# Optimization experiments

Measured on AMD Instinct MI355X. Metric: run time of the kernel, lower is better.

Reference implementation:

```python
import jax, jax.numpy as jnp
import numpy as np

IOU_HI = 0.5
IOU_LO = 0.0
ROI_BS = 256
POS_RATIO = 0.25
BG = 20  # background class id; valid classes 0..BG-1
NUM_POS = int(ROI_BS * POS_RATIO)
DELTAS_SCALING = np.array([10.0, 10.0, 5.0, 5.0], dtype=np.float32)  # (x, y, w, h)


def _make_boxes(key, shape):
    ka, kb = jax.random.split(key)
    c = jax.random.uniform(ka, shape + (2,), minval=0.05, maxval=0.95)
    s = jax.random.uniform(kb, shape + (2,), minval=0.02, maxval=0.4)
    lo = jnp.clip(c - s / 2, 0.0, 1.0)
    hi = jnp.clip(c + s / 2, 0.0, 1.0)
    return jnp.concatenate([lo, hi], -1)  # (y1, x1, y2, x2), normalized


def setup_inputs() -> dict:
    key = jax.random.key(0)
    k1, k2, k3 = jax.random.split(key, 3)
    B, N, G = 32, 12000, 200
    rois = _make_boxes(k1, (B, N))
    gt_boxes = _make_boxes(k2, (B, G))
    # class == BG marks a padded / invalid GT box
    gt_class_ids = jax.random.randint(k3, (B, G), 0, BG + 1).astype(jnp.int32)
    return {"rois": rois, "gt_class_ids": gt_class_ids, "gt_boxes": gt_boxes}


def _iou(rois, gts):
    # rois [N,4], gts [G,4] in (y1,x1,y2,x2) -> [N,G]
    y1 = jnp.maximum(rois[:, None, 0], gts[None, :, 0])
    x1 = jnp.maximum(rois[:, None, 1], gts[None, :, 1])
    y2 = jnp.minimum(rois[:, None, 2], gts[None, :, 2])
    x2 = jnp.minimum(rois[:, None, 3], gts[None, :, 3])
    inter = jnp.clip(y2 - y1, 0.0) * jnp.clip(x2 - x1, 0.0)
    ar = (rois[:, 2] - rois[:, 0]) * (rois[:, 3] - rois[:, 1])
    ag = (gts[:, 2] - gts[:, 0]) * (gts[:, 3] - gts[:, 1])
    return inter / (ar[:, None] + ag[None, :] - inter + 1e-8)


def _encode(r, g):
    # (tx, ty, tw, th) * scaling, r/g: [K,4] in (y1,x1,y2,x2)
    eps = 1e-6
    rh = r[:, 2] - r[:, 0]; rw = r[:, 3] - r[:, 1]
    rcy = r[:, 0] + rh / 2; rcx = r[:, 1] + rw / 2
    gh = g[:, 2] - g[:, 0]; gw = g[:, 3] - g[:, 1]
    gcy = g[:, 0] + gh / 2; gcx = g[:, 1] + gw / 2
    tx = (gcx - rcx) / (rw + eps)
    ty = (gcy - rcy) / (rh + eps)
    tw = jnp.log(jnp.maximum(gw, eps) / (rw + eps))
    th = jnp.log(jnp.maximum(gh, eps) / (rh + eps))
    return jnp.stack([tx, ty, tw, th], -1) * jnp.asarray(DELTAS_SCALING)


def _per_image(rois, gt_cls, gt_boxes):
    iou = _iou(rois, gt_boxes)                       # [N,G]
    valid_gt = gt_cls < BG
    iou = jnp.where(valid_gt[None, :], iou, -1.0)
    max_iou = iou.max(1)                             # [N]
    best_gt = iou.argmax(1)                          # [N]
    pos = max_iou >= IOU_HI
    neg = (max_iou < IOU_HI) & (max_iou >= IOU_LO)

    # deterministic sampling: highest-IoU positives / negatives first
    pos_val, pos_idx = jax.lax.top_k(jnp.where(pos, max_iou, -1.0), NUM_POS)
    pos_ok = pos_val > 0.0
    neg_val, neg_idx = jax.lax.top_k(jnp.where(neg, max_iou + 2.0, -1.0), ROI_BS)
    neg_ok = neg_val > 0.0

    rP = jnp.arange(NUM_POS, dtype=jnp.float32)
    rN = jnp.arange(ROI_BS, dtype=jnp.float32)
    prio = jnp.concatenate([jnp.where(pos_ok, 1e9 - rP, -1e9 - rP),
                            jnp.where(neg_ok, 1e6 - rN, -1e6 - rN)])
    cand_idx = jnp.concatenate([pos_idx, neg_idx])
    cand_pos = jnp.concatenate([pos_ok, jnp.zeros(ROI_BS, bool)])
    _, sel = jax.lax.top_k(prio, ROI_BS)
    sel_roi = cand_idx[sel]                          # [ROI_BS]
    sel_is_pos = cand_pos[sel]                       # [ROI_BS]

    labels = jnp.where(sel_is_pos, gt_cls[best_gt[sel_roi]], BG)
    rois_sel = rois[sel_roi]                         # [ROI_BS,4]
    gts_sel = gt_boxes[best_gt[sel_roi]]             # [ROI_BS,4]
    t = _encode(rois_sel, gts_sel) * sel_is_pos[:, None].astype(rois.dtype)

    cls_onehot = jax.nn.one_hot(labels, BG + 1, dtype=rois.dtype)   # [ROI_BS,BG+1]
    onehot_fg = jax.nn.one_hot(labels, BG, dtype=rois.dtype)        # zero row for bg
    mask4 = jnp.repeat(onehot_fg, 4, axis=1)                        # [ROI_BS,4*BG]
    deltas_full = (onehot_fg[:, :, None] * t[:, None, :]).reshape(ROI_BS, 4 * BG)
    reg = jnp.concatenate([mask4, deltas_full], -1)                 # [ROI_BS,8*BG]
    return rois_sel, cls_onehot, reg


def reference(rois, gt_class_ids, gt_boxes):
    return jax.vmap(_per_image)(rois, gt_class_ids, gt_boxes)
```

## Files before the change

### kernel.cpp

```cpp
#include <hip/hip_runtime.h>
#include <stdint.h>

#pragma clang fp contract(off)

#define BATCH 32
#define NROI  12000
#define NGT   200
#define BGCLS 20
#define ROIBS 256
#define NPOS  64
#define NBIN  1024
#define CAP   1024
#define TSEL  1024
#define HSH   16
#define HST   (NBIN + 2)

__device__ __forceinline__ void roi_maxiou_all(const float4* cbox, const float* carea,
                                               int nv, float ry1, float rx1,
                                               float ry2, float rx2,
                                               float& best, int& bj) {
#pragma clang fp contract(off)
  float ar = (ry2 - ry1) * (rx2 - rx1);
  best = -1.0f; bj = 0;
  for (int j = 0; j < nv; ++j) {
    float4 q = cbox[j];
    float yy1 = fmaxf(ry1, q.x);
    float xx1 = fmaxf(rx1, q.y);
    float yy2 = fminf(ry2, q.z);
    float xx2 = fminf(rx2, q.w);
    float inter = fmaxf(yy2 - yy1, 0.0f) * fmaxf(xx2 - xx1, 0.0f);
    float den = ((ar + carea[j]) - inter) + 1e-8f;
    float iou = inter / den;
    if (iou > best) { best = iou; bj = j; }
  }
}

__global__ __launch_bounds__(256) void k_ioumax(const float* __restrict__ rois,
                                                const int* __restrict__ gtc,
                                                const float* __restrict__ gtb,
                                                float* __restrict__ max_iou,
                                                int* __restrict__ best_j) {
#pragma clang fp contract(off)
  __shared__ float4 cbox[NGT];
  __shared__ float carea[NGT];
  __shared__ int snv, wtmp[4];
  const int b = blockIdx.y;
  const int tid = threadIdx.x;

  {
    bool valid = false; float4 p = make_float4(0.f, 0.f, 0.f, 0.f);
    if (tid < NGT) {
      p = *(const float4*)(gtb + ((size_t)b * NGT + tid) * 4);
      valid = gtc[(size_t)b * NGT + tid] < BGCLS;
    }
    unsigned long long m = __ballot(valid);
    int w = tid >> 6;
    if ((tid & 63) == 0) wtmp[w] = __popcll(m);
    __syncthreads();
    if (tid == 0) snv = wtmp[0] + wtmp[1] + wtmp[2] + wtmp[3];
    if (valid) {
      int off = 0;
      for (int i = 0; i < w; ++i) off += wtmp[i];
      int pos = off + __popcll(m & ((1ull << (tid & 63)) - 1ull));
      cbox[pos] = p;
      carea[pos] = (p.z - p.x) * (p.w - p.y);
    }
    __syncthreads();
  }
  const int nv = snv;

  int n = blockIdx.x * 256 + tid;
  if (n >= NROI) return;
  const float4 r = *(const float4*)(rois + ((size_t)b * NROI + n) * 4);
  const float ar = (r.z - r.x) * (r.w - r.y);

  float best; int bj;
  if (nv == 0) {
    best = -1.0f; bj = 0;
  } else {
    float v1 = -1.0f, v2 = -2.0f; int j1 = 0;
#pragma unroll 2
    for (int j = 0; j < nv; ++j) {
      float4 q = cbox[j];
      float ag = carea[j];
      float yy1 = fmaxf(r.x, q.x);
      float xx1 = fmaxf(r.y, q.y);
      float yy2 = fminf(r.z, q.z);
      float xx2 = fminf(r.w, q.w);
      float inter = fmaxf(yy2 - yy1, 0.0f) * fmaxf(xx2 - xx1, 0.0f);
      float den = ((ar + ag) - inter) + 1e-8f;
      float a = inter * __builtin_amdgcn_rcpf(den);
      bool gt = a > v1;
      v2 = gt ? v1 : fmaxf(v2, a);
      j1 = gt ? j : j1;
      v1 = gt ? a : v1;
    }
    if (v2 >= v1 * 0.999995f) {
      roi_maxiou_all(cbox, carea, nv, r.x, r.y, r.z, r.w, best, bj);
    } else {
      float4 q = cbox[j1];
      float yy1 = fmaxf(r.x, q.x);
      float xx1 = fmaxf(r.y, q.y);
      float yy2 = fminf(r.z, q.z);
      float xx2 = fminf(r.w, q.w);
      float inter = fmaxf(yy2 - yy1, 0.0f) * fmaxf(xx2 - xx1, 0.0f);
      float den = ((ar + carea[j1]) - inter) + 1e-8f;
      best = inter / den;
      bj = j1;
    }
  }
  max_iou[(size_t)b * NROI + n] = best;
  best_j[(size_t)b * NROI + n] = bj;
}

template <bool USE_WS>
__global__ __launch_bounds__(TSEL) void k_sel(const float* __restrict__ rois,
                                              const int* __restrict__ gtc,
                                              const float* __restrict__ gtb,
                                              const float* __restrict__ max_iou,
                                              const int* __restrict__ best_j,
                                              float* __restrict__ out) {
#pragma clang fp contract(off)
  __shared__ float4 cbox[NGT];
  __shared__ float carea[NGT];
  __shared__ int ccls[NGT];
  __shared__ int snv, wtmp[16];
  __shared__ int wtot[16], wnext[16];
  __shared__ float val[NROI];
  __shared__ unsigned long long list[CAP];
  __shared__ int hs[HSH][HST];
  __shared__ int ss[NBIN];
  __shared__ int sel_r[ROIBS];
  __shared__ int scnt, sT;
  const int b = blockIdx.x;
  const int tid = threadIdx.x;

  {
    bool valid = false; float4 p = make_float4(0.f, 0.f, 0.f, 0.f); int cls = BGCLS;
    if (tid < NGT) {
      p = *(const float4*)(gtb + ((size_t)b * NGT + tid) * 4);
      cls = gtc[(size_t)b * NGT + tid];
      valid = (cls < BGCLS);
    }
    unsigned long long m = __ballot(valid);
    int w = tid >> 6;
    if ((tid & 63) == 0) wtmp[w] = __popcll(m);
    if (tid < ROIBS) sel_r[tid] = 0;
    __syncthreads();
    if (tid == 0) { int s = 0; for (int i = 0; i < 16; ++i) s += wtmp[i]; snv = s; }
    if (valid) {
      int off = 0;
      for (int i = 0; i < w; ++i) off += wtmp[i];
      int pos = off + __popcll(m & ((1ull << (tid & 63)) - 1ull));
      cbox[pos] = p;
      carea[pos] = (p.z - p.x) * (p.w - p.y);
      ccls[pos] = cls;
    }
    __syncthreads();
  }
  const int nv = snv;

  if constexpr (USE_WS) {
    for (int n = tid; n < NROI; n += TSEL) val[n] = max_iou[(size_t)b * NROI + n];
  } else {
    for (int n = tid; n < NROI; n += TSEL) {
      const float4 r = *(const float4*)(rois + ((size_t)b * NROI + n) * 4);
      float best; int bj;
      roi_maxiou_all(cbox, carea, nv, r.x, r.y, r.z, r.w, best, bj);
      val[n] = best;
    }
  }
  __syncthreads();

  auto phase = [&](bool isPos, int need, unsigned base, int shift,
                   float lo, float hi, int slotBase) -> int {
    for (int i = tid; i < HSH * HST; i += TSEL) ((int*)hs)[i] = 0;
    if (tid == 0) { scnt = 0; sT = 0; }
    __syncthreads();
    const int sh = tid & (HSH - 1);
    for (int n = tid; n < NROI; n += TSEL) {
      float v = val[n];
      if (v >= lo && v < hi) {
        float kv = isPos ? v : (v + 2.0f);
        int bin = min((int)((__float_as_uint(kv) - base) >> shift), NBIN - 1);
        atomicAdd(&hs[sh][bin], 1);
      }
    }
    __syncthreads();
    int cnt_bin = 0;
#pragma unroll
    for (int i = 0; i < HSH; ++i) cnt_bin += hs[i][tid];
    const int lane = tid & 63, w = tid >> 6;
    int sfx = cnt_bin;
#pragma unroll
    for (int off = 1; off < 64; off <<= 1) {
      int t = __shfl_down(sfx, off, 64);
      sfx += (lane + off < 64) ? t : 0;
    }
    if (lane == 0) wtot[w] = sfx;
    __syncthreads();
    if (tid < 16) {
      int s = 0;
      for (int i = tid + 1; i < 16; ++i) s += wtot[i];
      wnext[tid] = s;
    }
    __syncthreads();
    const int suffix = sfx + wnext[w];
    ss[tid] = suffix;
    __syncthreads();
    {
      int nxt = (tid + 1 < NBIN) ? ss[tid + 1] : 0;
      if (suffix >= need && nxt < need) sT = tid;
    }
    __syncthreads();
    const int T = sT;
    for (int n = tid; n < NROI; n += TSEL) {
      float v = val[n];
      if (v >= lo && v < hi) {
        unsigned kh = __float_as_uint(isPos ? v : (v + 2.0f));
        int bin = min((int)((kh - base) >> shift), NBIN - 1);
        if (bin >= T) {
          int idx = atomicAdd(&scnt, 1);
          if (idx < CAP)
            list[idx] = ((unsigned long long)kh << 32) | (unsigned)(0x7fffffff - n);
        }
      }
    }
    __syncthreads();
    const int cnt = min(scnt, CAP);
    const int limit = min(cnt, need);
    if (tid < cnt) {
      unsigned long long ki = list[tid];
      int rank = 0;
      for (int j = 0; j < cnt; ++j) rank += (list[j] > ki);
      if (rank < limit)
        sel_r[slotBase + rank] = 0x7fffffff - (int)(ki & 0xffffffffu);
    }
    __syncthreads();
    return limit;
  };

  const int P = phase(true, NPOS, 0x3F000000u, 13, 0.5f, 3.0f, 0);
  phase(false, ROIBS - P, 0x40000000u, 11, 0.0f, 0.5f, P);

  {
    const int slot = tid >> 2, q = tid & 3;
    const int r = sel_r[slot];
    const int isp = (slot < P) ? 1 : 0;
    const float4 rv = *(const float4*)(rois + ((size_t)b * NROI + r) * 4);
    float ry1 = rv.x, rx1 = rv.y, ry2 = rv.z, rx2 = rv.w;
    int bj;
    if constexpr (USE_WS) {
      bj = best_j[(size_t)b * NROI + r];
    } else {
      float bb;
      roi_maxiou_all(cbox, carea, nv, ry1, rx1, ry2, rx2, bb, bj);
    }
    int label = isp ? ccls[bj] : BGCLS;

    float* out1 = out;
    float* out2 = out + (size_t)BATCH * ROIBS * 4;
    float* out3 = out + (size_t)BATCH * ROIBS * 25;
    size_t row = (size_t)b * ROIBS + slot;

    if (q == 0) {
      *(float4*)(out1 + row * 4) = rv;
      float* o2 = out2 + row * 21;
      for (int c = 0; c <= BGCLS; ++c) o2[c] = (c == label) ? 1.0f : 0.0f;
    }

    float t0 = 0.f, t1 = 0.f, t2 = 0.f, t3 = 0.f;
    if (isp) {
      const float eps = 1e-6f;
      float4 g = cbox[bj];
      float gy1 = g.x, gx1 = g.y, gy2 = g.z, gx2 = g.w;
      float rh = ry2 - ry1, rw = rx2 - rx1;
      float rcy = ry1 + rh * 0.5f, rcx = rx1 + rw * 0.5f;
      float gh = gy2 - gy1, gw = gx2 - gx1;
      float gcy = gy1 + gh * 0.5f, gcx = gx1 + gw * 0.5f;
      t0 = ((gcx - rcx) / (rw + eps)) * 10.0f;
      t1 = ((gcy - rcy) / (rh + eps)) * 10.0f;
      t2 = logf(fmaxf(gw, eps) / (rw + eps)) * 5.0f;
      t3 = logf(fmaxf(gh, eps) / (rh + eps)) * 5.0f;
    }
    int m0 = label * 4;
    float* o3 = out3 + row * 160;
    for (int c = q * 10; c < q * 10 + 10; ++c) {
      float4 wv = make_float4(0.f, 0.f, 0.f, 0.f);
      if (isp) {
        float* wp = &wv.x;
#pragma unroll
        for (int jj = 0; jj < 4; ++jj) {
          int e = c * 4 + jj;
          float x = 0.f;
          if (e >= m0 && e < m0 + 4) x = 1.0f;
          int d = e - 80 - m0;
          if (d == 0) x = t0; else if (d == 1) x = t1;
          else if (d == 2) x = t2; else if (d == 3) x = t3;
          wp[jj] = x;
        }
      }
      *(float4*)(o3 + c * 4) = wv;
    }
  }
}

extern "C" void kernel_launch(void* const* d_in, const int* in_sizes, int n_in,
                              void* d_out, int out_size, void* d_ws, size_t ws_size,
                              hipStream_t stream) {
  const float* rois = (const float*)d_in[0];
  const int*   gtc  = (const int*)d_in[1];
  const float* gtb  = (const float*)d_in[2];
  float*       out  = (float*)d_out;

  size_t need = (size_t)BATCH * NROI * 8;
  if (d_ws && ws_size >= need) {
    float* mi = (float*)d_ws;
    int*   bj = (int*)d_ws + (size_t)BATCH * NROI;
    k_ioumax<<<dim3((NROI + 255) / 256, BATCH), 256, 0, stream>>>(rois, gtc, gtb, mi, bj);
    k_sel<true><<<BATCH, TSEL, 0, stream>>>(rois, gtc, gtb, mi, bj, out);
  } else {
    k_sel<false><<<BATCH, TSEL, 0, stream>>>(rois, gtc, gtb, nullptr, nullptr, out);
  }
}
```

Baseline: 86.33 us.

## Process two ROIs per thread in IoU kernel, keep IoU values in registers

Result: slower. 89.53 us (+3.7%).

```diff
diff --git a/kernel.cpp b/kernel.cpp
--- a/kernel.cpp
+++ b/kernel.cpp
@@ -12,8 +12,11 @@
 #define NBIN  1024
 #define CAP   1024
 #define TSEL  1024
+#define VPT2  12
 #define HSH   16
 #define HST   (NBIN + 2)
+#define RPT   2
+#define IOBLK (256 * RPT)
 
 __device__ __forceinline__ void roi_maxiou_all(const float4* cbox, const float* carea,
                                                int nv, float ry1, float rx1,
@@ -35,11 +38,11 @@
   }
 }
 
-__global__ __launch_bounds__(256) void k_ioumax(const float* __restrict__ rois,
-                                                const int* __restrict__ gtc,
-                                                const float* __restrict__ gtb,
-                                                float* __restrict__ max_iou,
-                                                int* __restrict__ best_j) {
+__global__ __launch_bounds__(256, 4) void k_ioumax(const float* __restrict__ rois,
+                                                   const int* __restrict__ gtc,
+                                                   const float* __restrict__ gtb,
+                                                   float* __restrict__ max_iou,
+                                                   int* __restrict__ best_j) {
 #pragma clang fp contract(off)
   __shared__ float4 cbox[NGT];
   __shared__ float carea[NGT];
@@ -68,49 +71,59 @@
     __syncthreads();
   }
   const int nv = snv;
-
-  int n = blockIdx.x * 256 + tid;
-  if (n >= NROI) return;
-  const float4 r = *(const float4*)(rois + ((size_t)b * NROI + n) * 4);
-  const float ar = (r.z - r.x) * (r.w - r.y);
-
-  float best; int bj;
-  if (nv == 0) {
-    best = -1.0f; bj = 0;
-  } else {
-    float v1 = -1.0f, v2 = -2.0f; int j1 = 0;
+  const int n0 = blockIdx.x * IOBLK + tid;
+
+  float4 rb[RPT]; float ar[RPT]; float v1[RPT], v2[RPT]; int j1[RPT];
+#pragma unroll
+  for (int k = 0; k < RPT; ++k) {
+    int n = n0 + (k << 8);
+    rb[k] = (n < NROI) ? *(const float4*)(rois + ((size_t)b * NROI + n) * 4)
+                       : make_float4(2.f, 2.f, 2.f, 2.f);
+    ar[k] = (rb[k].z - rb[k].x) * (rb[k].w - rb[k].y);
+    v1[k] = -1.0f; v2[k] = -2.0f; j1[k] = 0;
+  }
 #pragma unroll 2
-    for (int j = 0; j < nv; ++j) {
-      float4 q = cbox[j];
-      float ag = carea[j];
-      float yy1 = fmaxf(r.x, q.x);
-      float xx1 = fmaxf(r.y, q.y);
-      float yy2 = fminf(r.z, q.z);
-      float xx2 = fminf(r.w, q.w);
+  for (int j = 0; j < nv; ++j) {
+    float4 q = cbox[j];
+    float ag = carea[j];
+#pragma unroll
+    for (int k = 0; k < RPT; ++k) {
+      float yy1 = fmaxf(rb[k].x, q.x);
+      float xx1 = fmaxf(rb[k].y, q.y);
+      float yy2 = fminf(rb[k].z, q.z);
+      float xx2 = fminf(rb[k].w, q.w);
       float inter = fmaxf(yy2 - yy1, 0.0f) * fmaxf(xx2 - xx1, 0.0f);
-      float den = ((ar + ag) - inter) + 1e-8f;
+      float den = ((ar[k] + ag) - inter) + 1e-8f;
       float a = inter * __builtin_amdgcn_rcpf(den);
-      bool gt = a > v1;
-      v2 = gt ? v1 : fmaxf(v2, a);
-      j1 = gt ? j : j1;
-      v1 = gt ? a : v1;
-    }
-    if (v2 >= v1 * 0.999995f) {
-      roi_maxiou_all(cbox, carea, nv, r.x, r.y, r.z, r.w, best, bj);
+      bool gt = a > v1[k];
+      v2[k] = gt ? v1[k] : fmaxf(v2[k], a);
+      j1[k] = gt ? j : j1[k];
+      v1[k] = gt ? a : v1[k];
+    }
+  }
+#pragma unroll
+  for (int k = 0; k < RPT; ++k) {
+    int n = n0 + (k << 8);
+    if (n >= NROI) continue;
+    float best; int bj;
+    if (nv == 0) {
+      best = -1.0f; bj = 0;
+    } else if (v2[k] >= v1[k] * 0.999995f) {
+      roi_maxiou_all(cbox, carea, nv, rb[k].x, rb[k].y, rb[k].z, rb[k].w, best, bj);
     } else {
-      float4 q = cbox[j1];
-      float yy1 = fmaxf(r.x, q.x);
-      float xx1 = fmaxf(r.y, q.y);
-      float yy2 = fminf(r.z, q.z);
-      float xx2 = fminf(r.w, q.w);
+      float4 q = cbox[j1[k]];
+      float yy1 = fmaxf(rb[k].x, q.x);
+      float xx1 = fmaxf(rb[k].y, q.y);
+      float yy2 = fminf(rb[k].z, q.z);
+      float xx2 = fminf(rb[k].w, q.w);
       float inter = fmaxf(yy2 - yy1, 0.0f) * fmaxf(xx2 - xx1, 0.0f);
-      float den = ((ar + carea[j1]) - inter) + 1e-8f;
+      float den = ((ar[k] + carea[j1[k]]) - inter) + 1e-8f;
       best = inter / den;
-      bj = j1;
-    }
-  }
-  max_iou[(size_t)b * NROI + n] = best;
-  best_j[(size_t)b * NROI + n] = bj;
+      bj = j1[k];
+    }
+    max_iou[(size_t)b * NROI + n] = best;
+    best_j[(size_t)b * NROI + n] = bj;
+  }
 }
 
 template <bool USE_WS>
@@ -126,7 +139,6 @@
   __shared__ int ccls[NGT];
   __shared__ int snv, wtmp[16];
   __shared__ int wtot[16], wnext[16];
-  __shared__ float val[NROI];
   __shared__ unsigned long long list[CAP];
   __shared__ int hs[HSH][HST];
   __shared__ int ss[NBIN];
@@ -134,6 +146,7 @@
   __shared__ int scnt, sT;
   const int b = blockIdx.x;
   const int tid = threadIdx.x;
+  const int lane = tid & 63;
 
   {
     bool valid = false; float4 p = make_float4(0.f, 0.f, 0.f, 0.f); int cls = BGCLS;
@@ -160,17 +173,21 @@
   }
   const int nv = snv;
 
-  if constexpr (USE_WS) {
-    for (int n = tid; n < NROI; n += TSEL) val[n] = max_iou[(size_t)b * NROI + n];
-  } else {
-    for (int n = tid; n < NROI; n += TSEL) {
-      const float4 r = *(const float4*)(rois + ((size_t)b * NROI + n) * 4);
-      float best; int bj;
-      roi_maxiou_all(cbox, carea, nv, r.x, r.y, r.z, r.w, best, bj);
-      val[n] = best;
-    }
-  }
-  __syncthreads();
+  float v[VPT2];
+#pragma unroll
+  for (int i = 0; i < VPT2; ++i) {
+    int n = tid + (i << 10);
+    if constexpr (USE_WS) {
+      v[i] = (n < NROI) ? max_iou[(size_t)b * NROI + n] : -3.0f;
+    } else {
+      if (n < NROI) {
+        const float4 r = *(const float4*)(rois + ((size_t)b * NROI + n) * 4);
+        float best; int bj;
+        roi_maxiou_all(cbox, carea, nv, r.x, r.y, r.z, r.w, best, bj);
+        v[i] = best;
+      } else v[i] = -3.0f;
+    }
+  }
 
   auto phase = [&](bool isPos, int need, unsigned base, int shift,
                    float lo, float hi, int slotBase) -> int {
@@ -178,10 +195,11 @@
     if (tid == 0) { scnt = 0; sT = 0; }
     __syncthreads();
     const int sh = tid & (HSH - 1);
-    for (int n = tid; n < NROI; n += TSEL) {
-      float v = val[n];
-      if (v >= lo && v < hi) {
-        float kv = isPos ? v : (v + 2.0f);
+#pragma unroll
+    for (int i = 0; i < VPT2; ++i) {
+      float x = v[i];
+      if (x >= lo && x < hi) {
+        float kv = isPos ? x : (x + 2.0f);
         int bin = min((int)((__float_as_uint(kv) - base) >> shift), NBIN - 1);
         atomicAdd(&hs[sh][bin], 1);
       }
@@ -190,7 +208,7 @@
     int cnt_bin = 0;
 #pragma unroll
     for (int i = 0; i < HSH; ++i) cnt_bin += hs[i][tid];
-    const int lane = tid & 63, w = tid >> 6;
+    const int w = tid >> 6;
     int sfx = cnt_bin;
 #pragma unroll
     for (int off = 1; off < 64; off <<= 1) {
@@ -214,16 +232,26 @@
     }
     __syncthreads();
     const int T = sT;
-    for (int n = tid; n < NROI; n += TSEL) {
-      float v = val[n];
-      if (v >= lo && v < hi) {
-        unsigned kh = __float_as_uint(isPos ? v : (v + 2.0f));
+#pragma unroll
+    for (int i = 0; i < VPT2; ++i) {
+      int n = tid + (i << 10);
+      float x = v[i];
+      bool pred = (x >= lo && x < hi);
+      unsigned kh = 0; 
+      if (pred) {
+        kh = __float_as_uint(isPos ? x : (x + 2.0f));
         int bin = min((int)((kh - base) >> shift), NBIN - 1);
-        if (bin >= T) {
-          int idx = atomicAdd(&scnt, 1);
-          if (idx < CAP)
-            list[idx] = ((unsigned long long)kh << 32) | (unsigned)(0x7fffffff - n);
-        }
+        pred = (bin >= T);
+      }
+      unsigned long long mk = __ballot(pred);
+      int c = __popcll(mk);
+      int bs = 0;
+      if (lane == 0 && c) bs = atomicAdd(&scnt, c);
+      bs = __shfl(bs, 0, 64);
+      if (pred) {
+        int idx = bs + __popcll(mk & ((1ull << lane) - 1ull));
+        if (idx < CAP)
+          list[idx] = ((unsigned long long)kh << 32) | (unsigned)(0x7fffffff - n);
       }
     }
     __syncthreads();
@@ -317,7 +345,7 @@
   if (d_ws && ws_size >= need) {
     float* mi = (float*)d_ws;
     int*   bj = (int*)d_ws + (size_t)BATCH * NROI;
-    k_ioumax<<<dim3((NROI + 255) / 256, BATCH), 256, 0, stream>>>(rois, gtc, gtb, mi, bj);
+    k_ioumax<<<dim3((NROI + IOBLK - 1) / IOBLK, BATCH), 256, 0, stream>>>(rois, gtc, gtb, mi, bj);
     k_sel<true><<<BATCH, TSEL, 0, stream>>>(rois, gtc, gtb, mi, bj, out);
   } else {
     k_sel<false><<<BATCH, TSEL, 0, stream>>>(rois, gtc, gtb, nullptr, nullptr, out);
```
